# Kernel tuning notes

Measured on AMD Instinct MI355X. Metric: run time of the kernel, lower is better.

The kernel has to match this reference:

```python
import jax, jax.numpy as jnp
import numpy as np

B, S, H = 2, 2048, 1024
NH, HD = 16, 64            # num heads, head dim
R = 8                      # lora rank
LORA_SCALE = 64.0 / 8.0    # lora_alpha / lora_rank
SCALE = jnp.sqrt(jnp.float32(HD))


def setup_inputs() -> dict:
    key = jax.random.key(0)
    ks = jax.random.split(key, 14)
    std = 1.0 / np.sqrt(H)
    p = {
        'hidden_states': jax.random.normal(ks[0], (B, S, H), jnp.float32),
        'attention_mask': jnp.ones((B, S), jnp.float32),
        # base projections, stored [in, out] so y = x @ W
        'Wq': jax.random.normal(ks[1], (H, H), jnp.float32) * std,
        'Wk': jax.random.normal(ks[2], (H, H), jnp.float32) * std,
        'Wv': jax.random.normal(ks[3], (H, H), jnp.float32) * std,
        'Wo': jax.random.normal(ks[4], (H, H), jnp.float32) * std,
        # LoRA down (A: [H,R]) / up (B: [R,H]) for q,k,v,output
        'Aq': jax.random.normal(ks[5], (H, R), jnp.float32) * 0.01,
        'Bq': jax.random.normal(ks[6], (R, H), jnp.float32) * 0.01,
        'Ak': jax.random.normal(ks[7], (H, R), jnp.float32) * 0.01,
        'Bk': jax.random.normal(ks[8], (R, H), jnp.float32) * 0.01,
        'Av': jax.random.normal(ks[9], (H, R), jnp.float32) * 0.01,
        'Bv': jax.random.normal(ks[10], (R, H), jnp.float32) * 0.01,
        'Ao': jax.random.normal(ks[11], (H, R), jnp.float32) * 0.01,
        'Bo': jax.random.normal(ks[12], (R, H), jnp.float32) * 0.01,
    }
    return p


def _heads(x):
    # [B,S,H] -> [B,NH,S,HD]
    return x.reshape(B, S, NH, HD).transpose(0, 2, 1, 3)


def reference(hidden_states, attention_mask, Wq, Wk, Wv, Wo,
              Aq, Bq, Ak, Bk, Av, Bv, Ao, Bo):
    hs = hidden_states
    sg = jax.lax.stop_gradient  # freeze_base=True: base projections are no_grad

    q = sg(hs @ Wq) + (hs @ Aq) @ Bq * LORA_SCALE
    k = sg(hs @ Wk) + (hs @ Ak) @ Bk * LORA_SCALE
    v = sg(hs @ Wv) + (hs @ Av) @ Bv * LORA_SCALE

    qh, kh, vh = _heads(q), _heads(k), _heads(v)  # [B,NH,S,HD]

    scores = jnp.einsum('bhqd,bhkd->bhqk', qh, kh) / SCALE  # [B,NH,S,S]
    mask = (1.0 - attention_mask)[:, None, None, :] * -10000.0
    scores = scores + mask
    probs = jax.nn.softmax(scores, axis=-1)  # dropout is identity in eval

    ctx = jnp.einsum('bhqk,bhkd->bhqd', probs, vh)
    ctx = ctx.transpose(0, 2, 1, 3).reshape(B, S, H)

    out = sg(ctx @ Wo) + (ctx @ Ao) @ Bo * LORA_SCALE
    return out
```

## Files before the change

### kernel.cpp

```cpp
#include <hip/hip_runtime.h>
#include <math.h>

typedef float fx4 __attribute__((ext_vector_type(4)));
typedef float f32x4 __attribute__((ext_vector_type(4)));
typedef float f32x16 __attribute__((ext_vector_type(16)));
typedef short bf16x8 __attribute__((ext_vector_type(8)));
typedef unsigned short us4 __attribute__((ext_vector_type(4)));
typedef unsigned short us8 __attribute__((ext_vector_type(8)));
typedef unsigned int u32x4 __attribute__((ext_vector_type(4)));

#define HDIM 1024
#define SEQ  2048
#define BATCH 2
#define NHEAD 16
#define HD    64
#define MTOT  4096
#define LSCALE 8.0f
#define LOG2E 1.44269504088896340736f

__device__ __forceinline__ unsigned short f2bf(float f) {
    union { float f; unsigned int u; } v; v.f = f;
    unsigned int r = v.u + 0x7FFFu + ((v.u >> 16) & 1u);
    return (unsigned short)(r >> 16);
}
__device__ __forceinline__ float bf2f(unsigned short h) {
    union { unsigned int u; float f; } v; v.u = ((unsigned int)h) << 16;
    return v.f;
}
__device__ __forceinline__ unsigned int cvt_pk_bf16(float a, float b) {
    unsigned int r;
    asm("v_cvt_pk_bf16_f32 %0, %1, %2" : "=v"(r) : "v"(a), "v"(b));
    return r;
}

__global__ __launch_bounds__(256)
void split_x_kernel(const float* __restrict__ X, unsigned short* __restrict__ Xh,
                    unsigned short* __restrict__ Xl, int n4)
{
    int i = blockIdx.x * 256 + threadIdx.x;
    int stride = gridDim.x * 256;
    for (; i < n4; i += stride) {
        fx4 v = *((const fx4*)X + i);
        us4 h, l;
#pragma unroll
        for (int j = 0; j < 4; ++j) {
            h[j] = f2bf(v[j]);
            l[j] = f2bf(v[j] - bf2f(h[j]));
        }
        *((us4*)Xh + i) = h;
        *((us4*)Xl + i) = l;
    }
}

__global__ __launch_bounds__(64)
void lora_down_kernel(const float* __restrict__ X,
                      const float* __restrict__ A0,
                      const float* __restrict__ A1,
                      const float* __restrict__ A2,
                      float* __restrict__ out, int nmat)
{
    int row  = blockIdx.x;
    int lane = threadIdx.x;
    const float* xr = X + (size_t)row * HDIM;
    float xv[16];
#pragma unroll
    for (int i = 0; i < 16; ++i) xv[i] = xr[lane + 64 * i];
    const float* Amats[3] = {A0, A1, A2};
    for (int m = 0; m < nmat; ++m) {
        const float* A = Amats[m];
        float s[8];
#pragma unroll
        for (int c = 0; c < 8; ++c) s[c] = 0.f;
#pragma unroll
        for (int i = 0; i < 16; ++i) {
            const float* ap = A + (size_t)(lane + 64 * i) * 8;
#pragma unroll
            for (int c = 0; c < 8; ++c) s[c] += xv[i] * ap[c];
        }
#pragma unroll
        for (int c = 0; c < 8; ++c) {
#pragma unroll
            for (int off = 1; off < 64; off <<= 1)
                s[c] += __shfl_xor(s[c], off, 64);
        }
        if (lane == 0) {
#pragma unroll
            for (int c = 0; c < 8; ++c)
                out[(size_t)row * 24 + m * 8 + c] = s[c];
        }
    }
}

__global__ __launch_bounds__(256)
void tsplit_w_kernel(const float* __restrict__ W0, const float* __restrict__ W1,
                     const float* __restrict__ W2, const float* __restrict__ W3,
                     unsigned short* __restrict__ WTbase)
{
    int z = blockIdx.z;
    const float* W = (z == 0) ? W0 : (z == 1) ? W1 : (z == 2) ? W2 : W3;
    unsigned short* WTh = WTbase + (size_t)z * 2097152;
    unsigned short* WTl = WTh + 1048576;
    int n0 = blockIdx.x * 64, k0 = blockIdx.y * 64;
    __shared__ unsigned int T[64][65];
    int t = threadIdx.x;
#pragma unroll
    for (int i = 0; i < 4; ++i) {
        int idx = t + 256 * i;
        int r = idx >> 4, c4 = (idx & 15) * 4;
        fx4 w = *(const fx4*)&W[(size_t)(k0 + r) * HDIM + n0 + c4];
#pragma unroll
        for (int j = 0; j < 4; ++j) {
            unsigned short hi = f2bf(w[j]);
            unsigned short lo = f2bf(w[j] - bf2f(hi));
            T[r][c4 + j] = (unsigned int)hi | ((unsigned int)lo << 16);
        }
    }
    __syncthreads();
#pragma unroll
    for (int i = 0; i < 4; ++i) {
        int idx = t + 256 * i;
        int n = idx >> 4, kg = (idx & 15) * 4;
        us4 hv, lv;
#pragma unroll
        for (int j = 0; j < 4; ++j) {
            unsigned int p = T[kg + j][n];
            hv[j] = (unsigned short)(p & 0xffffu);
            lv[j] = (unsigned short)(p >> 16);
        }
        *(us4*)&WTh[(size_t)(n0 + n) * HDIM + k0 + kg] = hv;
        *(us4*)&WTl[(size_t)(n0 + n) * HDIM + k0 + kg] = lv;
    }
}

__global__ __launch_bounds__(256)
void transpose_v_kernel(const unsigned short* __restrict__ vb,
                        unsigned short* __restrict__ vt)
{
    int s0 = blockIdx.x * 64;
    int bh = blockIdx.y;
    int b = bh >> 4, h = bh & 15;
    __shared__ unsigned short T[64][80];
    int t = threadIdx.x;
#pragma unroll
    for (int i = 0; i < 2; ++i) {
        int u = t + 256 * i;
        int r = u >> 3, cg = u & 7;
        us8 v = *(const us8*)&vb[(size_t)(b * SEQ + s0 + r) * HDIM + h * HD + 8 * cg];
        *(us8*)&T[r][8 * cg] = v;
    }
    __syncthreads();
#pragma unroll
    for (int i = 0; i < 2; ++i) {
        int u = t + 256 * i;
        int d = u & 63, sg = u >> 6;
        us8 v;
#pragma unroll
        for (int j = 0; j < 8; ++j) v[j] = T[8 * sg + j][d];
        *(us8*)&vt[(size_t)(bh * HD + d) * SEQ + s0 + 8 * sg] = v;
    }
}

__global__ __launch_bounds__(64)
void lora_down_bf_kernel(const unsigned short* __restrict__ Xh,
                         const unsigned short* __restrict__ Xl,
                         const float* __restrict__ A,
                         float* __restrict__ out)
{
    int row  = blockIdx.x;
    int lane = threadIdx.x;
    const unsigned short* xh = Xh + (size_t)row * HDIM;
    const unsigned short* xl = Xl + (size_t)row * HDIM;
    float xv[16];
#pragma unroll
    for (int i = 0; i < 16; ++i)
        xv[i] = bf2f(xh[lane + 64 * i]) + bf2f(xl[lane + 64 * i]);
    float s[8];
#pragma unroll
    for (int c = 0; c < 8; ++c) s[c] = 0.f;
#pragma unroll
    for (int i = 0; i < 16; ++i) {
        const float* ap = A + (size_t)(lane + 64 * i) * 8;
#pragma unroll
        for (int c = 0; c < 8; ++c) s[c] += xv[i] * ap[c];
    }
#pragma unroll
    for (int c = 0; c < 8; ++c) {
#pragma unroll
        for (int off = 1; off < 64; off <<= 1)
            s[c] += __shfl_xor(s[c], off, 64);
    }
    if (lane == 0) {
#pragma unroll
        for (int c = 0; c < 8; ++c) out[(size_t)row * 8 + c] = s[c];
    }
}

template<bool OUTF32, int BM, int ZM>
__global__ __launch_bounds__(256, BM == 128 ? 2 : 3)
void gemm_mfma_kernel(const unsigned short* __restrict__ Xh,
                      const unsigned short* __restrict__ WTbase, int wsel0,
                      const float* __restrict__ XA, int xa_stride, int xa_off0,
                      const float* __restrict__ Bu0, const float* __restrict__ Bu1, const float* __restrict__ Bu2,
                      void* __restrict__ O0, void* __restrict__ O1, void* __restrict__ O2)
{
    constexpr int FN = (BM == 128) ? 4 : 2;
    int pz, byy;
    if (ZM > 1) { pz = blockIdx.y % ZM; byy = blockIdx.y / ZM; }
    else        { pz = blockIdx.z;      byy = blockIdx.y; }
    const unsigned short* WTh = WTbase + (size_t)(wsel0 + pz) * 2097152;
    const unsigned short* WTl = WTh + 1048576;
    const float* Bu = (pz == 0) ? Bu0 : (pz == 1) ? Bu1 : Bu2;
    void* Ovp       = (pz == 0) ? O0 : (pz == 1) ? O1 : O2;
    int xa_off = xa_off0 + pz * 8;

    int brow = byy * BM, bcol = blockIdx.x * 128;
    int t = threadIdx.x, wid = t >> 6, lane = t & 63, l15 = lane & 15, g = lane >> 4;
    int wm = (BM == 128) ? (wid >> 1) * 64 : 0;
    int wn = (BM == 128) ? (wid & 1) * 64 : wid * 32;

    __shared__ unsigned short Ah[BM][40];
    __shared__ unsigned short Bh[128][40];
    __shared__ unsigned short Bl[128][40];

    f32x4 acc[4][FN];
#pragma unroll
    for (int i = 0; i < 4; ++i)
#pragma unroll
        for (int j = 0; j < FN; ++j) acc[i][j] = (f32x4){0.f, 0.f, 0.f, 0.f};

    int sm = t >> 2, skg = t & 3;
    const unsigned short* aH0 = Xh  + (size_t)(brow + sm) * HDIM + 8 * skg;
    const unsigned short* bH0 = WTh + (size_t)(bcol + sm) * HDIM + 8 * skg;
    const unsigned short* bL0 = WTl + (size_t)(bcol + sm) * HDIM + 8 * skg;
    const size_t R64 = (size_t)64 * HDIM;

    us8 rAH0, rAH1, rBH0, rBH1, rBL0, rBL1;
    rAH0 = *(const us8*)(aH0);
    if (BM == 128) rAH1 = *(const us8*)(aH0 + R64);
    rBH0 = *(const us8*)(bH0);
    rBH1 = *(const us8*)(bH0 + R64);
    rBL0 = *(const us8*)(bL0);
    rBL1 = *(const us8*)(bL0 + R64);

    for (int k0 = 0; k0 < HDIM; k0 += 32) {
        __syncthreads();
        *(us8*)&Ah[sm][8 * skg] = rAH0;
        if (BM == 128)
            *(us8*)&Ah[(sm + 64) & (BM - 1)][8 * skg] = rAH1;
        *(us8*)&Bh[sm][8 * skg]      = rBH0;
        *(us8*)&Bh[sm + 64][8 * skg] = rBH1;
        *(us8*)&Bl[sm][8 * skg]      = rBL0;
        *(us8*)&Bl[sm + 64][8 * skg] = rBL1;
        __syncthreads();
        if (k0 + 32 < HDIM) {
            int ko = k0 + 32;
            rAH0 = *(const us8*)(aH0 + ko);
            if (BM == 128) rAH1 = *(const us8*)(aH0 + R64 + ko);
            rBH0 = *(const us8*)(bH0 + ko);
            rBH1 = *(const us8*)(bH0 + R64 + ko);
            rBL0 = *(const us8*)(bL0 + ko);
            rBL1 = *(const us8*)(bL0 + R64 + ko);
        }
        bf16x8 fah[4], fbh[FN], fbl[FN];
#pragma unroll
        for (int f = 0; f < 4; ++f)
            fah[f] = *(const bf16x8*)&Ah[wm + 16 * f + l15][8 * g];
#pragma unroll
        for (int f = 0; f < FN; ++f) {
            fbh[f] = *(const bf16x8*)&Bh[wn + 16 * f + l15][8 * g];
            fbl[f] = *(const bf16x8*)&Bl[wn + 16 * f + l15][8 * g];
        }
#pragma unroll
        for (int fm = 0; fm < 4; ++fm)
#pragma unroll
            for (int fn = 0; fn < FN; ++fn) {
                f32x4 a = acc[fm][fn];
                a = __builtin_amdgcn_mfma_f32_16x16x32_bf16(fah[fm], fbh[fn], a, 0, 0, 0);
                a = __builtin_amdgcn_mfma_f32_16x16x32_bf16(fah[fm], fbl[fn], a, 0, 0, 0);
                acc[fm][fn] = a;
            }
    }

    float lb[8][FN];
#pragma unroll
    for (int rr = 0; rr < 8; ++rr)
#pragma unroll
        for (int fn = 0; fn < FN; ++fn)
            lb[rr][fn] = Bu[(size_t)rr * HDIM + bcol + wn + 16 * fn + l15] * LSCALE;

#pragma unroll
    for (int fm = 0; fm < 4; ++fm) {
        float la[4][8];
#pragma unroll
        for (int r = 0; r < 4; ++r) {
            int row = brow + wm + 16 * fm + 4 * g + r;
            const float* lap = XA + (size_t)row * xa_stride + xa_off;
            fx4 q0 = *(const fx4*)lap;
            fx4 q1 = *(const fx4*)(lap + 4);
#pragma unroll
            for (int j = 0; j < 4; ++j) { la[r][j] = q0[j]; la[r][4 + j] = q1[j]; }
        }
#pragma unroll
        for (int fn = 0; fn < FN; ++fn)
#pragma unroll
            for (int r = 0; r < 4; ++r) {
                float sum = acc[fm][fn][r];
#pragma unroll
                for (int rr = 0; rr < 8; ++rr) sum += la[r][rr] * lb[rr][fn];
                size_t row = (size_t)(brow + wm + 16 * fm + 4 * g + r);
                int col = bcol + wn + 16 * fn + l15;
                if (OUTF32) ((float*)Ovp)[row * HDIM + col] = sum;
                else ((unsigned short*)Ovp)[row * HDIM + col] = f2bf(sum);
            }
    }
}

#define QBLK 128
#define KVB  64
#define NT   (SEQ / KVB)

__global__ __launch_bounds__(256, 2)
void attn_mfma_kernel(const unsigned short* __restrict__ Qg, const unsigned short* __restrict__ Kg,
                      const unsigned short* __restrict__ Vt, const float* __restrict__ mask,
                      unsigned short* __restrict__ Ch, unsigned short* __restrict__ Cl)
{
    int qt = blockIdx.x, hd = blockIdx.y, b = blockIdx.z;
    int t    = threadIdx.x;
    int wid  = t >> 6;
    int lane = t & 63;
    int q31  = lane & 31;
    int g1   = lane >> 5;

    __shared__ __align__(16) unsigned short Ks[2][64][72];
    __shared__ __align__(16) unsigned short Vs[2][64][72];
    __shared__ __align__(16) float Msd[2][64];

    bf16x8 qB[4];
    const unsigned short* qp = Qg + (size_t)(b * SEQ + qt * QBLK + wid * 32 + q31) * HDIM + hd * HD;
#pragma unroll
    for (int kc = 0; kc < 4; ++kc)
        qB[kc] = *(const bf16x8*)(qp + 16 * kc + 8 * g1);

    float m0 = 0.f;
    f32x4 l4 = (f32x4){0.f, 0.f, 0.f, 0.f};
    f32x16 accO[2];
#pragma unroll
    for (int dh = 0; dh < 2; ++dh)
#pragma unroll
        for (int i = 0; i < 16; ++i) accO[dh][i] = 0.f;

    const unsigned short* kp0 = Kg + (size_t)(b * SEQ) * HDIM + hd * HD;
    const unsigned short* vt0 = Vt + (size_t)((b * NHEAD + hd) * HD) * SEQ;

    const float QSCL = 0.125f * LOG2E;
    const float MSCL = -10000.0f * LOG2E;

    int r0 = t >> 3,           c0 = (t & 7) * 8;
    int r1 = (t + 256) >> 3,   c1 = c0;

    *(us8*)&Ks[0][r0][c0] = *(const us8*)(kp0 + (size_t)r0 * HDIM + c0);
    *(us8*)&Ks[0][r1][c1] = *(const us8*)(kp0 + (size_t)r1 * HDIM + c1);
    *(us8*)&Vs[0][r0][c0] = *(const us8*)(vt0 + (size_t)r0 * SEQ + c0);
    *(us8*)&Vs[0][r1][c1] = *(const us8*)(vt0 + (size_t)r1 * SEQ + c1);
    if (t < 64) Msd[0][t] = (1.0f - mask[b * SEQ + t]) * MSCL;
    __syncthreads();

    int cur = 0;
    for (int kt = 0; kt < NT; ++kt) {
        us8 knr0, knr1, vnr0, vnr1;
        float mreg = 1.0f;
        bool more = (kt + 1 < NT);
        if (more) {
            const unsigned short* kp = kp0 + (size_t)(kt + 1) * KVB * HDIM;
            const unsigned short* vp = vt0 + (kt + 1) * KVB;
            knr0 = *(const us8*)(kp + (size_t)r0 * HDIM + c0);
            knr1 = *(const us8*)(kp + (size_t)r1 * HDIM + c1);
            vnr0 = *(const us8*)(vp + (size_t)r0 * SEQ + c0);
            vnr1 = *(const us8*)(vp + (size_t)r1 * SEQ + c1);
            if (t < 64) mreg = mask[b * SEQ + (kt + 1) * KVB + t];
        }

        f32x16 sQ[2];
#pragma unroll
        for (int kvh = 0; kvh < 2; ++kvh) {
            f32x16 a;
#pragma unroll
            for (int i = 0; i < 16; ++i) a[i] = 0.f;
#pragma unroll
            for (int kc = 0; kc < 4; ++kc) {
                bf16x8 kA = *(const bf16x8*)&Ks[cur][32 * kvh + q31][16 * kc + 8 * g1];
                a = __builtin_amdgcn_mfma_f32_32x32x16_bf16(kA, qB[kc], a, 0, 0, 0);
            }
            sQ[kvh] = a;
        }

#pragma unroll
        for (int kvh = 0; kvh < 2; ++kvh)
#pragma unroll
            for (int hh = 0; hh < 4; ++hh) {
                fx4 msk = *(const fx4*)&Msd[cur][32 * kvh + 8 * hh + 4 * g1];
#pragma unroll
                for (int r = 0; r < 4; ++r)
                    sQ[kvh][4 * hh + r] = fmaf(sQ[kvh][4 * hh + r], QSCL, msk[r]);
            }

        if (kt == 0) {
            float mx = sQ[0][0];
#pragma unroll
            for (int kvh = 0; kvh < 2; ++kvh)
#pragma unroll
                for (int i = 0; i < 16; ++i) mx = fmaxf(mx, sQ[kvh][i]);
            mx = fmaxf(mx, __shfl_xor(mx, 32, 64));
            m0 = fmaxf(mx, -64.f);
        }

#pragma unroll
        for (int kvh = 0; kvh < 2; ++kvh)
#pragma unroll
            for (int hh = 0; hh < 4; ++hh)
#pragma unroll
                for (int r = 0; r < 4; ++r) {
                    float p = exp2f(sQ[kvh][4 * hh + r] - m0);
                    sQ[kvh][4 * hh + r] = p;
                    l4[r] += p;
                }

        unsigned int pkx[2][4], pky[2][4];
#pragma unroll
        for (int kvh = 0; kvh < 2; ++kvh)
#pragma unroll
            for (int hh = 0; hh < 4; ++hh) {
                pkx[kvh][hh] = cvt_pk_bf16(sQ[kvh][4 * hh + 0], sQ[kvh][4 * hh + 1]);
                pky[kvh][hh] = cvt_pk_bf16(sQ[kvh][4 * hh + 2], sQ[kvh][4 * hh + 3]);
            }

        bf16x8 pB[4];
#pragma unroll
        for (int kvh = 0; kvh < 2; ++kvh)
#pragma unroll
            for (int kc2 = 0; kc2 < 2; ++kc2) {
                unsigned int x0 = pkx[kvh][2 * kc2], x1 = pkx[kvh][2 * kc2 + 1];
                unsigned int y0 = pky[kvh][2 * kc2], y1 = pky[kvh][2 * kc2 + 1];
                asm("v_permlane32_swap_b32 %0, %1" : "+v"(x0), "+v"(x1));
                asm("v_permlane32_swap_b32 %0, %1" : "+v"(y0), "+v"(y1));
                u32x4 dd;
                dd[0] = x0; dd[1] = y0; dd[2] = x1; dd[3] = y1;
                pB[2 * kvh + kc2] = *(bf16x8*)&dd;
            }

#pragma unroll
        for (int dh = 0; dh < 2; ++dh) {
            f32x16 a = accO[dh];
#pragma unroll
            for (int kcp = 0; kcp < 4; ++kcp) {
                bf16x8 vA = *(const bf16x8*)&Vs[cur][32 * dh + q31][16 * kcp + 8 * g1];
                a = __builtin_amdgcn_mfma_f32_32x32x16_bf16(vA, pB[kcp], a, 0, 0, 0);
            }
            accO[dh] = a;
        }

        if (more) {
            *(us8*)&Ks[cur ^ 1][r0][c0] = knr0;
            *(us8*)&Ks[cur ^ 1][r1][c1] = knr1;
            *(us8*)&Vs[cur ^ 1][r0][c0] = vnr0;
            *(us8*)&Vs[cur ^ 1][r1][c1] = vnr1;
            if (t < 64) Msd[cur ^ 1][t] = (1.0f - mreg) * MSCL;
        }
        __syncthreads();
        cur ^= 1;
    }

    float l = (l4[0] + l4[1]) + (l4[2] + l4[3]);
    l += __shfl_xor(l, 32, 64);
    float inv = 1.0f / l;
    size_t row = (size_t)(b * SEQ + qt * QBLK + wid * 32 + q31);
#pragma unroll
    for (int dh = 0; dh < 2; ++dh)
#pragma unroll
        for (int hh = 0; hh < 4; ++hh) {
            us4 hv, lv;
#pragma unroll
            for (int r = 0; r < 4; ++r) {
                float o = accO[dh][4 * hh + r] * inv;
                unsigned short hi = f2bf(o);
                hv[r] = hi;
                lv[r] = f2bf(o - bf2f(hi));
            }
            size_t idx = row * HDIM + hd * HD + 32 * dh + 8 * hh + 4 * g1;
            *(us4*)&Ch[idx] = hv;
            *(us4*)&Cl[idx] = lv;
        }
}

extern "C" void kernel_launch(void* const* d_in, const int* in_sizes, int n_in,
                              void* d_out, int out_size, void* d_ws, size_t ws_size,
                              hipStream_t stream)
{
    const float* hs   = (const float*)d_in[0];
    const float* mask = (const float*)d_in[1];
    const float* Wq = (const float*)d_in[2];
    const float* Wk = (const float*)d_in[3];
    const float* Wv = (const float*)d_in[4];
    const float* Wo = (const float*)d_in[5];
    const float* Aq = (const float*)d_in[6];
    const float* Bq = (const float*)d_in[7];
    const float* Ak = (const float*)d_in[8];
    const float* Bk = (const float*)d_in[9];
    const float* Av = (const float*)d_in[10];
    const float* Bv = (const float*)d_in[11];
    const float* Ao = (const float*)d_in[12];
    const float* Bo = (const float*)d_in[13];
    float* out = (float*)d_out;

    char* w = (char*)d_ws;
    unsigned short* Xh = (unsigned short*)(w);
    unsigned short* Xl = (unsigned short*)(w + ((size_t)8 << 20));
    unsigned short* WT = (unsigned short*)(w + ((size_t)16 << 20));
    unsigned short* qb = (unsigned short*)(w + ((size_t)32 << 20));
    unsigned short* kb = (unsigned short*)(w + ((size_t)40 << 20));
    unsigned short* vb = (unsigned short*)(w + ((size_t)48 << 20));
    unsigned short* vt = (unsigned short*)(w + ((size_t)56 << 20));
    float* hsA  = (float*)(w + ((size_t)64 << 20));
    float* ctxA = (float*)(w + ((size_t)64 << 20) + 400 * 1024);

    split_x_kernel<<<2048, 256, 0, stream>>>(hs, Xh, Xl, MTOT * HDIM / 4);
    tsplit_w_kernel<<<dim3(16, 16, 4), 256, 0, stream>>>(Wq, Wk, Wv, Wo, WT);
    lora_down_kernel<<<MTOT, 64, 0, stream>>>(hs, Aq, Ak, Av, hsA, 3);
    gemm_mfma_kernel<false, 128, 3><<<dim3(8, 96), 256, 0, stream>>>(
        Xh, WT, 0, hsA, 24, 0, Bq, Bk, Bv, qb, kb, vb);
    transpose_v_kernel<<<dim3(SEQ / 64, BATCH * NHEAD), 256, 0, stream>>>(vb, vt);
    attn_mfma_kernel<<<dim3(SEQ / QBLK, NHEAD, BATCH), 256, 0, stream>>>(
        qb, kb, vt, mask, Xh , Xl );
    lora_down_bf_kernel<<<MTOT, 64, 0, stream>>>(Xh, Xl, Ao, ctxA);
    gemm_mfma_kernel<true, 64, 1><<<dim3(8, 64, 1), 256, 0, stream>>>(
        Xh, WT, 3, ctxA, 8, 0, Bo, Bo, Bo, out, out, out);
}
```

Measured before the change: 197.2 us.

## Split attention KV sequence across two wave groups and merge partial softmax results

The attention block grows to 512 threads. Two halves of four waves each process half of the key/value tiles, with their own double-buffered LDS tiles. At the end, half 1 writes its partial output, row sums and max through LDS, and half 0 merges them flash-decoding style before writing the context. This raises parallelism per query tile to hide memory and MFMA latency, at the cost of doubled LDS, a merge step and extra barriers shared by both halves.

```diff
diff --git a/kernel.cpp b/kernel.cpp
--- a/kernel.cpp
+++ b/kernel.cpp
@@ -317,9 +317,9 @@
 
 #define QBLK 128
 #define KVB  64
-#define NT   (SEQ / KVB)
-
-__global__ __launch_bounds__(256, 2)
+#define NTH  16
+
+__global__ __launch_bounds__(512, 4)
 void attn_mfma_kernel(const unsigned short* __restrict__ Qg, const unsigned short* __restrict__ Kg,
                       const unsigned short* __restrict__ Vt, const float* __restrict__ mask,
                       unsigned short* __restrict__ Ch, unsigned short* __restrict__ Cl)
@@ -327,16 +327,19 @@
     int qt = blockIdx.x, hd = blockIdx.y, b = blockIdx.z;
     int t    = threadIdx.x;
     int wid  = t >> 6;
+    int half = wid >> 2;
+    int wq   = wid & 3;
     int lane = t & 63;
     int q31  = lane & 31;
     int g1   = lane >> 5;
-
-    __shared__ __align__(16) unsigned short Ks[2][64][72];
-    __shared__ __align__(16) unsigned short Vs[2][64][72];
-    __shared__ __align__(16) float Msd[2][64];
+    int th   = t & 255;
+
+    __shared__ __align__(16) unsigned short Ks[2][2][64][72];
+    __shared__ __align__(16) unsigned short Vs[2][2][64][72];
+    __shared__ __align__(16) float Msd[2][2][64];
 
     bf16x8 qB[4];
-    const unsigned short* qp = Qg + (size_t)(b * SEQ + qt * QBLK + wid * 32 + q31) * HDIM + hd * HD;
+    const unsigned short* qp = Qg + (size_t)(b * SEQ + qt * QBLK + wq * 32 + q31) * HDIM + hd * HD;
 #pragma unroll
     for (int kc = 0; kc < 4; ++kc)
         qB[kc] = *(const bf16x8*)(qp + 16 * kc + 8 * g1);
@@ -355,29 +358,35 @@
     const float QSCL = 0.125f * LOG2E;
     const float MSCL = -10000.0f * LOG2E;
 
-    int r0 = t >> 3,           c0 = (t & 7) * 8;
-    int r1 = (t + 256) >> 3,   c1 = c0;
-
-    *(us8*)&Ks[0][r0][c0] = *(const us8*)(kp0 + (size_t)r0 * HDIM + c0);
-    *(us8*)&Ks[0][r1][c1] = *(const us8*)(kp0 + (size_t)r1 * HDIM + c1);
-    *(us8*)&Vs[0][r0][c0] = *(const us8*)(vt0 + (size_t)r0 * SEQ + c0);
-    *(us8*)&Vs[0][r1][c1] = *(const us8*)(vt0 + (size_t)r1 * SEQ + c1);
-    if (t < 64) Msd[0][t] = (1.0f - mask[b * SEQ + t]) * MSCL;
+    int rA = th >> 3, c0 = (th & 7) * 8;
+    int rB = rA + 32;
+    int kb = half * NTH;
+
+    {
+        const unsigned short* kp = kp0 + (size_t)(kb * KVB) * HDIM;
+        const unsigned short* vp = vt0 + kb * KVB;
+        *(us8*)&Ks[half][0][rA][c0] = *(const us8*)(kp + (size_t)rA * HDIM + c0);
+        *(us8*)&Ks[half][0][rB][c0] = *(const us8*)(kp + (size_t)rB * HDIM + c0);
+        *(us8*)&Vs[half][0][rA][c0] = *(const us8*)(vp + (size_t)rA * SEQ + c0);
+        *(us8*)&Vs[half][0][rB][c0] = *(const us8*)(vp + (size_t)rB * SEQ + c0);
+        if (th < 64) Msd[half][0][th] = (1.0f - mask[b * SEQ + kb * KVB + th]) * MSCL;
+    }
     __syncthreads();
 
     int cur = 0;
-    for (int kt = 0; kt < NT; ++kt) {
+    for (int ktl = 0; ktl < NTH; ++ktl) {
+        int kt = kb + ktl;
         us8 knr0, knr1, vnr0, vnr1;
         float mreg = 1.0f;
-        bool more = (kt + 1 < NT);
+        bool more = (ktl + 1 < NTH);
         if (more) {
             const unsigned short* kp = kp0 + (size_t)(kt + 1) * KVB * HDIM;
             const unsigned short* vp = vt0 + (kt + 1) * KVB;
-            knr0 = *(const us8*)(kp + (size_t)r0 * HDIM + c0);
-            knr1 = *(const us8*)(kp + (size_t)r1 * HDIM + c1);
-            vnr0 = *(const us8*)(vp + (size_t)r0 * SEQ + c0);
-            vnr1 = *(const us8*)(vp + (size_t)r1 * SEQ + c1);
-            if (t < 64) mreg = mask[b * SEQ + (kt + 1) * KVB + t];
+            knr0 = *(const us8*)(kp + (size_t)rA * HDIM + c0);
+            knr1 = *(const us8*)(kp + (size_t)rB * HDIM + c0);
+            vnr0 = *(const us8*)(vp + (size_t)rA * SEQ + c0);
+            vnr1 = *(const us8*)(vp + (size_t)rB * SEQ + c0);
+            if (th < 64) mreg = mask[b * SEQ + (kt + 1) * KVB + th];
         }
 
         f32x16 sQ[2];
@@ -388,7 +397,7 @@
             for (int i = 0; i < 16; ++i) a[i] = 0.f;
 #pragma unroll
             for (int kc = 0; kc < 4; ++kc) {
-                bf16x8 kA = *(const bf16x8*)&Ks[cur][32 * kvh + q31][16 * kc + 8 * g1];
+                bf16x8 kA = *(const bf16x8*)&Ks[half][cur][32 * kvh + q31][16 * kc + 8 * g1];
                 a = __builtin_amdgcn_mfma_f32_32x32x16_bf16(kA, qB[kc], a, 0, 0, 0);
             }
             sQ[kvh] = a;
@@ -398,13 +407,13 @@
         for (int kvh = 0; kvh < 2; ++kvh)
 #pragma unroll
             for (int hh = 0; hh < 4; ++hh) {
-                fx4 msk = *(const fx4*)&Msd[cur][32 * kvh + 8 * hh + 4 * g1];
+                fx4 msk = *(const fx4*)&Msd[half][cur][32 * kvh + 8 * hh + 4 * g1];
 #pragma unroll
                 for (int r = 0; r < 4; ++r)
                     sQ[kvh][4 * hh + r] = fmaf(sQ[kvh][4 * hh + r], QSCL, msk[r]);
             }
 
-        if (kt == 0) {
+        if (ktl == 0) {
             float mx = sQ[0][0];
 #pragma unroll
             for (int kvh = 0; kvh < 2; ++kvh)
@@ -453,18 +462,18 @@
             f32x16 a = accO[dh];
 #pragma unroll
             for (int kcp = 0; kcp < 4; ++kcp) {
-                bf16x8 vA = *(const bf16x8*)&Vs[cur][32 * dh + q31][16 * kcp + 8 * g1];
+                bf16x8 vA = *(const bf16x8*)&Vs[half][cur][32 * dh + q31][16 * kcp + 8 * g1];
                 a = __builtin_amdgcn_mfma_f32_32x32x16_bf16(vA, pB[kcp], a, 0, 0, 0);
             }
             accO[dh] = a;
         }
 
         if (more) {
-            *(us8*)&Ks[cur ^ 1][r0][c0] = knr0;
-            *(us8*)&Ks[cur ^ 1][r1][c1] = knr1;
-            *(us8*)&Vs[cur ^ 1][r0][c0] = vnr0;
-            *(us8*)&Vs[cur ^ 1][r1][c1] = vnr1;
-            if (t < 64) Msd[cur ^ 1][t] = (1.0f - mreg) * MSCL;
+            *(us8*)&Ks[half][cur ^ 1][rA][c0] = knr0;
+            *(us8*)&Ks[half][cur ^ 1][rB][c0] = knr1;
+            *(us8*)&Vs[half][cur ^ 1][rA][c0] = vnr0;
+            *(us8*)&Vs[half][cur ^ 1][rB][c0] = vnr1;
+            if (th < 64) Msd[half][cur ^ 1][th] = (1.0f - mreg) * MSCL;
         }
         __syncthreads();
         cur ^= 1;
@@ -472,24 +481,52 @@
 
     float l = (l4[0] + l4[1]) + (l4[2] + l4[3]);
     l += __shfl_xor(l, 32, 64);
-    float inv = 1.0f / l;
-    size_t row = (size_t)(b * SEQ + qt * QBLK + wid * 32 + q31);
-#pragma unroll
-    for (int dh = 0; dh < 2; ++dh)
-#pragma unroll
-        for (int hh = 0; hh < 4; ++hh) {
-            us4 hv, lv;
-#pragma unroll
-            for (int r = 0; r < 4; ++r) {
-                float o = accO[dh][4 * hh + r] * inv;
-                unsigned short hi = f2bf(o);
-                hv[r] = hi;
-                lv[r] = f2bf(o - bf2f(hi));
-            }
-            size_t idx = row * HDIM + hd * HD + 32 * dh + 8 * hh + 4 * g1;
-            *(us4*)&Ch[idx] = hv;
-            *(us4*)&Cl[idx] = lv;
-        }
+
+    float* CB = (float*)&Ks[0][0][0][0];
+    float* CL = (float*)&Vs[0][0][0][0];
+    if (half == 1) {
+        int base = (wq * 64 + lane) * 36;
+#pragma unroll
+        for (int dh = 0; dh < 2; ++dh)
+#pragma unroll
+            for (int q4 = 0; q4 < 4; ++q4) {
+                f32x4 v;
+#pragma unroll
+                for (int r = 0; r < 4; ++r) v[r] = accO[dh][4 * q4 + r];
+                *(f32x4*)&CB[base + dh * 16 + 4 * q4] = v;
+            }
+        CL[wq * 64 + lane] = l;
+        CL[256 + wq * 64 + lane] = m0;
+    }
+    __syncthreads();
+
+    if (half == 0) {
+        int base = (wq * 64 + lane) * 36;
+        float mB = CL[256 + wq * 64 + lane];
+        float lB = CL[wq * 64 + lane];
+        float M  = fmaxf(m0, mB);
+        float sA = exp2f(m0 - M);
+        float sB = exp2f(mB - M);
+        float inv = 1.0f / (l * sA + lB * sB);
+        size_t row = (size_t)(b * SEQ + qt * QBLK + wq * 32 + q31);
+#pragma unroll
+        for (int dh = 0; dh < 2; ++dh)
+#pragma unroll
+            for (int hh = 0; hh < 4; ++hh) {
+                f32x4 ob = *(const f32x4*)&CB[base + dh * 16 + 4 * hh];
+                us4 hv, lv;
+#pragma unroll
+                for (int r = 0; r < 4; ++r) {
+                    float o = (accO[dh][4 * hh + r] * sA + ob[r] * sB) * inv;
+                    unsigned short hi = f2bf(o);
+                    hv[r] = hi;
+                    lv[r] = f2bf(o - bf2f(hi));
+                }
+                size_t idx = row * HDIM + hd * HD + 32 * dh + 8 * hh + 4 * g1;
+                *(us4*)&Ch[idx] = hv;
+                *(us4*)&Cl[idx] = lv;
+            }
+    }
 }
 
 extern "C" void kernel_launch(void* const* d_in, const int* in_sizes, int n_in,
@@ -529,7 +566,7 @@
     gemm_mfma_kernel<false, 128, 3><<<dim3(8, 96), 256, 0, stream>>>(
         Xh, WT, 0, hsA, 24, 0, Bq, Bk, Bv, qb, kb, vb);
     transpose_v_kernel<<<dim3(SEQ / 64, BATCH * NHEAD), 256, 0, stream>>>(vb, vt);
-    attn_mfma_kernel<<<dim3(SEQ / QBLK, NHEAD, BATCH), 256, 0, stream>>>(
+    attn_mfma_kernel<<<dim3(SEQ / QBLK, NHEAD, BATCH), 512, 0, stream>>>(
         qb, kb, vt, mask, Xh , Xl );
     lora_down_bf_kernel<<<MTOT, 64, 0, stream>>>(Xh, Xl, Ao, ctxA);
     gemm_mfma_kernel<true, 64, 1><<<dim3(8, 64, 1), 256, 0, stream>>>(
```

Measured after the change: 211.5 us. +7.3%, slower.
